# Performance work log

Hardware: AMD Instinct MI355X
Metric: run time of the kernel (lower is better)

Reference implementation:

```python
import jax, jax.numpy as jnp
import numpy as np

B, IN, H = 64, 1024, 1024

def _lin(x, W, b):
    # torch nn.Linear: y = x @ W.T + b, W:[out,in]
    return x @ W.T + b

def setup_inputs() -> dict:
    key = jax.random.key(0)
    ks = jax.random.split(key, 16)
    s_in = 1.0 / np.sqrt(IN)
    s_cat = 1.0 / np.sqrt(IN + H)
    s_h = 1.0 / np.sqrt(H)
    return {
        "x": jax.random.normal(ks[0], (B, IN), jnp.float32),
        "h": jax.random.normal(ks[1], (B, H), jnp.float32),
        "C": jax.random.normal(ks[2], (B, H, H), jnp.float32) * 0.02,
        "Wq": jax.random.normal(ks[3], (H, IN), jnp.float32) * s_in,
        "bq": jax.random.normal(ks[4], (H,), jnp.float32) * s_in,
        "Wk": jax.random.normal(ks[5], (H, IN), jnp.float32) * s_in,
        "bk": jax.random.normal(ks[6], (H,), jnp.float32) * s_in,
        "Wv": jax.random.normal(ks[7], (H, IN), jnp.float32) * s_in,
        "bv": jax.random.normal(ks[8], (H,), jnp.float32) * s_in,
        "Wf": jax.random.normal(ks[9], (H, IN + H), jnp.float32) * s_cat,
        "bf": jax.random.normal(ks[10], (H,), jnp.float32) * s_cat,
        "Wi": jax.random.normal(ks[11], (H, IN + H), jnp.float32) * s_cat,
        "bi": jax.random.normal(ks[12], (H,), jnp.float32) * s_cat,
        "Wo": jax.random.normal(ks[13], (H, H), jnp.float32) * s_h,
        "bo": jax.random.normal(ks[14], (H,), jnp.float32) * s_h,
    }

def reference(x, h, C, Wq, bq, Wk, bk, Wv, bv, Wf, bf, Wi, bi, Wo, bo):
    q = _lin(x, Wq, bq)            # [B,H]
    k = _lin(x, Wk, bk)            # [B,H]
    v = _lin(x, Wv, bv)            # [B,H]
    combined = jnp.concatenate([x, h], axis=-1)       # [B,IN+H]
    f = jax.nn.sigmoid(_lin(combined, Wf, bf))        # [B,H]
    i = jax.nn.sigmoid(_lin(combined, Wi, bi))        # [B,H]
    # gated matrix-memory update: C_new[b,m,n] = f[b,m]*C[b,m,n] + i[b,m]*k[b,m]*v[b,n]
    C_new = f[:, :, None] * C + (i * k)[:, :, None] * v[:, None, :]
    # readout: matvec with q then tanh and output projection
    r = jnp.einsum('bmn,bn->bm', C_new, q)            # [B,H]
    h_new = _lin(jnp.tanh(r), Wo, bo)                 # [B,H]
    return (h_new, C_new)
```

## Files before the change

### kernel.cpp

```cpp
#include <hip/hip_runtime.h>
#include <math.h>

#define HB 64
#define HD 1024
#define KSF 256
#define KSB 128
#define XS 68

typedef float f32x4 __attribute__((ext_vector_type(4)));

template<int KS>
__device__ __forceinline__ void splitk_tile(
    const float* __restrict__ X0, int noff,
    const float* __restrict__ W, int K,
    int m0, int k0,
    float* __restrict__ P)
{
    __shared__ __align__(16) float Xs[32][XS];
    __shared__ __align__(16) float Ws[32][XS];
    const int t  = threadIdx.x;
    const int bx = t & 15;
    const int my = t >> 4;
    float acc[4][4] = {};

    float4 xp[2], wp[2];
    #pragma unroll
    for (int i = 0; i < 2; ++i) {
        int u = t + 256 * i;
        int r = u >> 3, nq = u & 7;
        xp[i] = *(const float4*)&X0[r * HD + (k0 - noff) + nq * 4];
        wp[i] = *(const float4*)&W[(long long)(m0 + r) * K + k0 + nq * 4];
    }

    for (int kc = 0; kc < KS; kc += 32) {
        #pragma unroll
        for (int i = 0; i < 2; ++i) {
            int u = t + 256 * i;
            int r = u >> 3, nq = u & 7;
            Xs[nq * 4 + 0][r] = xp[i].x; Xs[nq * 4 + 1][r] = xp[i].y;
            Xs[nq * 4 + 2][r] = xp[i].z; Xs[nq * 4 + 3][r] = xp[i].w;
            Ws[nq * 4 + 0][r] = wp[i].x; Ws[nq * 4 + 1][r] = wp[i].y;
            Ws[nq * 4 + 2][r] = wp[i].z; Ws[nq * 4 + 3][r] = wp[i].w;
        }
        __syncthreads();
        if (kc + 32 < KS) {
            const int n0 = k0 + kc + 32;
            #pragma unroll
            for (int i = 0; i < 2; ++i) {
                int u = t + 256 * i;
                int r = u >> 3, nq = u & 7;
                xp[i] = *(const float4*)&X0[r * HD + (n0 - noff) + nq * 4];
                wp[i] = *(const float4*)&W[(long long)(m0 + r) * K + n0 + nq * 4];
            }
        }
        #pragma unroll
        for (int n = 0; n < 32; ++n) {
            float4 xv = *(const float4*)&Xs[n][bx * 4];
            float4 wv = *(const float4*)&Ws[n][my * 4];
            float xe[4] = {xv.x, xv.y, xv.z, xv.w};
            float we[4] = {wv.x, wv.y, wv.z, wv.w};
            #pragma unroll
            for (int i = 0; i < 4; ++i)
                #pragma unroll
                for (int j = 0; j < 4; ++j)
                    acc[i][j] = fmaf(xe[i], we[j], acc[i][j]);
        }
        __syncthreads();
    }
    #pragma unroll
    for (int i = 0; i < 4; ++i) {
        float4 o4 = make_float4(acc[i][0], acc[i][1], acc[i][2], acc[i][3]);
        *(float4*)&P[(bx * 4 + i) * HD + m0 + my * 4] = o4;
    }
}

__global__ __launch_bounds__(256) void qkvfi_splitk(
    const float* __restrict__ x, const float* __restrict__ h,
    const float* __restrict__ Wq, const float* __restrict__ Wk,
    const float* __restrict__ Wv, const float* __restrict__ Wf,
    const float* __restrict__ Wi, float* __restrict__ P)
{
    const int gy = blockIdx.y;
    const float* W; int K, split;
    if (gy < 12) {
        int g = gy >> 2; split = gy & 3; K = HD;
        W = (g == 0) ? Wq : (g == 1) ? Wk : Wv;
    } else {
        int tt = gy - 12; int g = tt >> 3; split = tt & 7; K = 2 * HD;
        W = g ? Wi : Wf;
    }
    const int k0 = split * KSF;
    const float* X0; int noff;
    if (k0 < HD) { X0 = x; noff = 0; } else { X0 = h; noff = HD; }
    splitk_tile<KSF>(X0, noff, W, K, blockIdx.x * 64, k0,
                     P + (size_t)gy * (HB * HD));
}

__global__ __launch_bounds__(256) void out_splitk(
    const float* __restrict__ tr, const float* __restrict__ Wo,
    float* __restrict__ P2)
{
    const int split = blockIdx.y;
    splitk_tile<KSB>(tr, 0, Wo, HD, blockIdx.x * 64, split * KSB,
                     P2 + (size_t)split * (HB * HD));
}

__global__ __launch_bounds__(256) void reduce_qkvfi(
    const float* __restrict__ P,
    const float* __restrict__ bq, const float* __restrict__ bk,
    const float* __restrict__ bv, const float* __restrict__ bfv,
    const float* __restrict__ biv,
    float* __restrict__ q, float* __restrict__ k, float* __restrict__ v,
    float* __restrict__ fg, float* __restrict__ ig)
{
    const int o4 = blockIdx.x * 256 + threadIdx.x;
    const int g  = o4 >> 14;
    const int r4 = o4 & 16383;
    const int m4 = r4 & 255;
    int base, ns, act; const float* bias; float* out;
    switch (g) {
        case 0:  base = 0;  ns = 4; bias = bq;  out = q;  act = 0; break;
        case 1:  base = 4;  ns = 4; bias = bk;  out = k;  act = 0; break;
        case 2:  base = 8;  ns = 4; bias = bv;  out = v;  act = 0; break;
        case 3:  base = 12; ns = 8; bias = bfv; out = fg; act = 1; break;
        default: base = 20; ns = 8; bias = biv; out = ig; act = 1; break;
    }
    float4 s = ((const float4*)bias)[m4];
    const float4* P4 = (const float4*)P;
    for (int i = 0; i < ns; ++i) {
        float4 p = P4[(size_t)(base + i) * 16384 + r4];
        s.x += p.x; s.y += p.y; s.z += p.z; s.w += p.w;
    }
    if (act) {
        s.x = 1.0f / (1.0f + expf(-s.x)); s.y = 1.0f / (1.0f + expf(-s.y));
        s.z = 1.0f / (1.0f + expf(-s.z)); s.w = 1.0f / (1.0f + expf(-s.w));
    }
    ((float4*)out)[r4] = s;
}

__global__ __launch_bounds__(256) void reduce_out(
    const float* __restrict__ P2, const float* __restrict__ bo,
    float* __restrict__ hnew)
{
    const int o4 = blockIdx.x * 256 + threadIdx.x;
    const int m4 = o4 & 255;
    float4 s = ((const float4*)bo)[m4];
    const float4* P4 = (const float4*)P2;
    #pragma unroll
    for (int i = 0; i < 8; ++i) {
        float4 p = P4[(size_t)i * 16384 + o4];
        s.x += p.x; s.y += p.y; s.z += p.z; s.w += p.w;
    }
    ((float4*)hnew)[o4] = s;
}

__global__ __launch_bounds__(256) void update_kernel(
    const float* __restrict__ C,
    const float* __restrict__ q, const float* __restrict__ k,
    const float* __restrict__ v, const float* __restrict__ fg,
    const float* __restrict__ ig,
    float* __restrict__ Cn, float* __restrict__ tr)
{
    __shared__ __align__(16) float qs[HD];
    __shared__ __align__(16) float vs[HD];
    const int t    = threadIdx.x;
    const int wid  = t >> 6;
    const int lane = t & 63;
    const int row  = blockIdx.x * 4 + wid;
    const int b    = row >> 10;
    const int m    = row & (HD - 1);

    ((float4*)qs)[t] = ((const float4*)q)[b * 256 + t];
    ((float4*)vs)[t] = ((const float4*)v)[b * 256 + t];

    const float fm  = fg[b * HD + m];
    const float ikm = ig[b * HD + m] * k[b * HD + m];
    __syncthreads();

    const f32x4* C4 = (const f32x4*)C;
    const f32x4* V4 = (const f32x4*)vs;
    const f32x4* Q4 = (const f32x4*)qs;
    f32x4*       N4 = (f32x4*)Cn;

    const int base = row * (HD / 4);

    float racc = 0.f;
    #pragma unroll
    for (int j = 0; j < 4; ++j) {
        int o = lane + 64 * j;
        f32x4 c4 = __builtin_nontemporal_load(&C4[base + o]);
        f32x4 v4 = V4[o];
        f32x4 q4 = Q4[o];
        f32x4 cn;
        cn.x = fmaf(fm, c4.x, ikm * v4.x);
        cn.y = fmaf(fm, c4.y, ikm * v4.y);
        cn.z = fmaf(fm, c4.z, ikm * v4.z);
        cn.w = fmaf(fm, c4.w, ikm * v4.w);
        N4[base + o] = cn;
        racc += cn.x * q4.x + cn.y * q4.y + cn.z * q4.z + cn.w * q4.w;
    }
    #pragma unroll
    for (int off = 32; off; off >>= 1) racc += __shfl_xor(racc, off);
    if (lane == 0) tr[row] = tanhf(racc);
}

extern "C" void kernel_launch(void* const* d_in, const int* in_sizes, int n_in,
                              void* d_out, int out_size, void* d_ws, size_t ws_size,
                              hipStream_t stream) {
    const float* x  = (const float*)d_in[0];
    const float* h  = (const float*)d_in[1];
    const float* C  = (const float*)d_in[2];
    const float* Wq = (const float*)d_in[3];
    const float* bq = (const float*)d_in[4];
    const float* Wk = (const float*)d_in[5];
    const float* bk = (const float*)d_in[6];
    const float* Wv = (const float*)d_in[7];
    const float* bv = (const float*)d_in[8];
    const float* Wf = (const float*)d_in[9];
    const float* bf = (const float*)d_in[10];
    const float* Wi = (const float*)d_in[11];
    const float* bi = (const float*)d_in[12];
    const float* Wo = (const float*)d_in[13];
    const float* bo = (const float*)d_in[14];

    float* outp = (float*)d_out;
    float* hnew = outp;
    float* Cn   = outp + HB * HD;

    const size_t SL = (size_t)HB * HD;
    float* ws = (float*)d_ws;
    float* q  = ws + 0 * SL;
    float* k  = ws + 1 * SL;
    float* v  = ws + 2 * SL;
    float* fg = ws + 3 * SL;
    float* ig = ws + 4 * SL;
    float* tr = ws + 5 * SL;
    float* P  = ws + 6 * SL;
    float* P2 = ws + 34 * SL;

    qkvfi_splitk<<<dim3(16, 28), 256, 0, stream>>>(x, h, Wq, Wk, Wv, Wf, Wi, P);
    reduce_qkvfi<<<dim3(320), 256, 0, stream>>>(P, bq, bk, bv, bf, bi,
                                                q, k, v, fg, ig);
    update_kernel<<<dim3((HB * HD) / 4), 256, 0, stream>>>(
        C, q, k, v, fg, ig, Cn, tr);
    out_splitk<<<dim3(16, 8), 256, 0, stream>>>(tr, Wo, P2);
    reduce_out<<<dim3(64), 256, 0, stream>>>(P2, bo, hnew);
}
```

Measured before the change: 124.0 us.

## Fuse split-K reductions into GEMM kernels via last-block atomic counters

Replaces the separate reduce kernels with a last-arriving-block pattern. Each split-K block bumps a per-tile atomic counter, and the final block for that tile sums the partials, adds the bias and applies the sigmoid where needed. This removes two kernel launches and their launch gaps. The counters are never reset, so the code uses modulo arithmetic to keep working across repeated calls, which assumes the workspace starts zeroed. The cost is extra threadfences and a serialized reduction tail in one block per tile.

```diff
diff --git a/kernel.cpp b/kernel.cpp
--- a/kernel.cpp
+++ b/kernel.cpp
@@ -74,84 +74,108 @@
     }
 }
 
-__global__ __launch_bounds__(256) void qkvfi_splitk(
+__global__ __launch_bounds__(256) void qkvfi_fused(
     const float* __restrict__ x, const float* __restrict__ h,
     const float* __restrict__ Wq, const float* __restrict__ Wk,
     const float* __restrict__ Wv, const float* __restrict__ Wf,
-    const float* __restrict__ Wi, float* __restrict__ P)
+    const float* __restrict__ Wi,
+    const float* __restrict__ bq, const float* __restrict__ bk,
+    const float* __restrict__ bv, const float* __restrict__ bfv,
+    const float* __restrict__ biv,
+    float* __restrict__ P,
+    float* __restrict__ q, float* __restrict__ k, float* __restrict__ v,
+    float* __restrict__ fg, float* __restrict__ ig,
+    unsigned int* __restrict__ cnt)
 {
     const int gy = blockIdx.y;
-    const float* W; int K, split;
+    const int mt = blockIdx.x;
+    const int m0 = mt * 64;
+    const float* W; int K, split, g;
     if (gy < 12) {
-        int g = gy >> 2; split = gy & 3; K = HD;
+        g = gy >> 2; split = gy & 3; K = HD;
         W = (g == 0) ? Wq : (g == 1) ? Wk : Wv;
     } else {
-        int tt = gy - 12; int g = tt >> 3; split = tt & 7; K = 2 * HD;
-        W = g ? Wi : Wf;
+        int tt = gy - 12; g = 3 + (tt >> 3); split = tt & 7; K = 2 * HD;
+        W = (g == 4) ? Wi : Wf;
     }
     const int k0 = split * KSF;
     const float* X0; int noff;
     if (k0 < HD) { X0 = x; noff = 0; } else { X0 = h; noff = HD; }
-    splitk_tile<KSF>(X0, noff, W, K, blockIdx.x * 64, k0,
-                     P + (size_t)gy * (HB * HD));
-}
-
-__global__ __launch_bounds__(256) void out_splitk(
+    splitk_tile<KSF>(X0, noff, W, K, m0, k0, P + (size_t)gy * (HB * HD));
+
+    const int nsplit = (g < 3) ? 4 : 8;
+    const int sb     = (g < 3) ? g * 4 : 12 + (g - 3) * 8;
+    __threadfence();
+    __shared__ unsigned int oldv;
+    if (threadIdx.x == 0) oldv = atomicAdd(&cnt[g * 16 + mt], 1u);
+    __syncthreads();
+    if (oldv % nsplit != (unsigned)(nsplit - 1)) return;
+    __threadfence();
+
+    const float* bias; float* out; int act;
+    switch (g) {
+        case 0:  bias = bq;  out = q;  act = 0; break;
+        case 1:  bias = bk;  out = k;  act = 0; break;
+        case 2:  bias = bv;  out = v;  act = 0; break;
+        case 3:  bias = bfv; out = fg; act = 1; break;
+        default: bias = biv; out = ig; act = 1; break;
+    }
+    const float4* P4 = (const float4*)P;
+    const int c0 = m0 / 4;
+    #pragma unroll
+    for (int it = 0; it < 4; ++it) {
+        const int u   = threadIdx.x + 256 * it;
+        const int b   = u >> 4;
+        const int c   = u & 15;
+        const int idx = b * 256 + c0 + c;
+        float4 s = ((const float4*)bias)[c0 + c];
+        for (int i = 0; i < nsplit; ++i) {
+            float4 p = P4[(size_t)(sb + i) * 16384 + idx];
+            s.x += p.x; s.y += p.y; s.z += p.z; s.w += p.w;
+        }
+        if (act) {
+            s.x = 1.0f / (1.0f + expf(-s.x)); s.y = 1.0f / (1.0f + expf(-s.y));
+            s.z = 1.0f / (1.0f + expf(-s.z)); s.w = 1.0f / (1.0f + expf(-s.w));
+        }
+        ((float4*)out)[idx] = s;
+    }
+}
+
+__global__ __launch_bounds__(256) void out_fused(
     const float* __restrict__ tr, const float* __restrict__ Wo,
-    float* __restrict__ P2)
-{
+    const float* __restrict__ bo,
+    float* __restrict__ P2, float* __restrict__ hnew,
+    unsigned int* __restrict__ cnt)
+{
+    const int mt    = blockIdx.x;
     const int split = blockIdx.y;
-    splitk_tile<KSB>(tr, 0, Wo, HD, blockIdx.x * 64, split * KSB,
+    const int m0    = mt * 64;
+    splitk_tile<KSB>(tr, 0, Wo, HD, m0, split * KSB,
                      P2 + (size_t)split * (HB * HD));
-}
-
-__global__ __launch_bounds__(256) void reduce_qkvfi(
-    const float* __restrict__ P,
-    const float* __restrict__ bq, const float* __restrict__ bk,
-    const float* __restrict__ bv, const float* __restrict__ bfv,
-    const float* __restrict__ biv,
-    float* __restrict__ q, float* __restrict__ k, float* __restrict__ v,
-    float* __restrict__ fg, float* __restrict__ ig)
-{
-    const int o4 = blockIdx.x * 256 + threadIdx.x;
-    const int g  = o4 >> 14;
-    const int r4 = o4 & 16383;
-    const int m4 = r4 & 255;
-    int base, ns, act; const float* bias; float* out;
-    switch (g) {
-        case 0:  base = 0;  ns = 4; bias = bq;  out = q;  act = 0; break;
-        case 1:  base = 4;  ns = 4; bias = bk;  out = k;  act = 0; break;
-        case 2:  base = 8;  ns = 4; bias = bv;  out = v;  act = 0; break;
-        case 3:  base = 12; ns = 8; bias = bfv; out = fg; act = 1; break;
-        default: base = 20; ns = 8; bias = biv; out = ig; act = 1; break;
-    }
-    float4 s = ((const float4*)bias)[m4];
-    const float4* P4 = (const float4*)P;
-    for (int i = 0; i < ns; ++i) {
-        float4 p = P4[(size_t)(base + i) * 16384 + r4];
-        s.x += p.x; s.y += p.y; s.z += p.z; s.w += p.w;
-    }
-    if (act) {
-        s.x = 1.0f / (1.0f + expf(-s.x)); s.y = 1.0f / (1.0f + expf(-s.y));
-        s.z = 1.0f / (1.0f + expf(-s.z)); s.w = 1.0f / (1.0f + expf(-s.w));
-    }
-    ((float4*)out)[r4] = s;
-}
-
-__global__ __launch_bounds__(256) void reduce_out(
-    const float* __restrict__ P2, const float* __restrict__ bo,
-    float* __restrict__ hnew)
-{
-    const int o4 = blockIdx.x * 256 + threadIdx.x;
-    const int m4 = o4 & 255;
-    float4 s = ((const float4*)bo)[m4];
+
+    __threadfence();
+    __shared__ unsigned int oldv;
+    if (threadIdx.x == 0) oldv = atomicAdd(&cnt[mt], 1u);
+    __syncthreads();
+    if (oldv % 8u != 7u) return;
+    __threadfence();
+
     const float4* P4 = (const float4*)P2;
-    #pragma unroll
-    for (int i = 0; i < 8; ++i) {
-        float4 p = P4[(size_t)i * 16384 + o4];
-        s.x += p.x; s.y += p.y; s.z += p.z; s.w += p.w;
-    }
-    ((float4*)hnew)[o4] = s;
+    const int c0 = m0 / 4;
+    #pragma unroll
+    for (int it = 0; it < 4; ++it) {
+        const int u   = threadIdx.x + 256 * it;
+        const int b   = u >> 4;
+        const int c   = u & 15;
+        const int idx = b * 256 + c0 + c;
+        float4 s = ((const float4*)bo)[c0 + c];
+        #pragma unroll
+        for (int i = 0; i < 8; ++i) {
+            float4 p = P4[(size_t)i * 16384 + idx];
+            s.x += p.x; s.y += p.y; s.z += p.z; s.w += p.w;
+        }
+        ((float4*)hnew)[idx] = s;
+    }
 }
 
 __global__ __launch_bounds__(256) void update_kernel(
@@ -237,12 +261,13 @@
     float* tr = ws + 5 * SL;
     float* P  = ws + 6 * SL;
     float* P2 = ws + 34 * SL;
-
-    qkvfi_splitk<<<dim3(16, 28), 256, 0, stream>>>(x, h, Wq, Wk, Wv, Wf, Wi, P);
-    reduce_qkvfi<<<dim3(320), 256, 0, stream>>>(P, bq, bk, bv, bf, bi,
-                                                q, k, v, fg, ig);
+    unsigned int* cnt  = (unsigned int*)(ws + 42 * SL);
+    unsigned int* cnt2 = cnt + 128;
+
+    qkvfi_fused<<<dim3(16, 28), 256, 0, stream>>>(
+        x, h, Wq, Wk, Wv, Wf, Wi, bq, bk, bv, bf, bi,
+        P, q, k, v, fg, ig, cnt);
     update_kernel<<<dim3((HB * HD) / 4), 256, 0, stream>>>(
         C, q, k, v, fg, ig, Cn, tr);
-    out_splitk<<<dim3(16, 8), 256, 0, stream>>>(tr, Wo, P2);
-    reduce_out<<<dim3(64), 256, 0, stream>>>(P2, bo, hnew);
-}
+    out_fused<<<dim3(16, 8), 256, 0, stream>>>(tr, Wo, bo, P2, hnew, cnt2);
+}
```

New measurement: 207.9 us. 67.6% more time.
